# Optimization experiments

Measured on AMD Instinct MI355X. Metric: run time of the kernel, lower is better.

The kernel has to match this reference:

```python
import jax, jax.numpy as jnp
import numpy as np

N, E, DIM, H, T, R = 50000, 400000, 128, 8, 4, 6
D = DIM // H  # head dim = 16


def setup_inputs() -> dict:
    key = jax.random.key(0)
    ks = jax.random.split(key, 12)
    s = 0.1
    return {
        "x": jax.random.normal(ks[0], (N, DIM), jnp.float32),
        "src": jax.random.randint(ks[1], (E,), 0, N),
        "dst": jax.random.randint(ks[2], (E,), 0, N),
        "ntype": jax.random.randint(ks[3], (N,), 0, T),
        "etype": jax.random.randint(ks[4], (E,), 0, R),
        # TypedLinear weights: [num_types, in, out] (no bias in DGL TypedLinear)
        "Wk": jax.random.normal(ks[5], (T, DIM, DIM), jnp.float32) * s,
        "Wq": jax.random.normal(ks[6], (T, DIM, DIM), jnp.float32) * s,
        "Wv": jax.random.normal(ks[7], (T, DIM, DIM), jnp.float32) * s,
        "Wa": jax.random.normal(ks[8], (T, DIM, DIM), jnp.float32) * s,
        # relation_pri[h][r], relation_att/msg: per-head per-etype [D,D]
        "rel_pri": jnp.ones((H, R), jnp.float32) + jax.random.normal(ks[9], (H, R), jnp.float32) * 0.1,
        "rel_att": jax.random.normal(ks[10], (H, R, D, D), jnp.float32) * 0.25,
        "rel_msg": jax.random.normal(ks[11], (H, R, D, D), jnp.float32) * 0.25,
        "skip": jnp.ones((T,), jnp.float32),  # sigmoid-gated skip per node type
        "ln_gamma": jnp.ones((DIM,), jnp.float32),
        "ln_beta": jnp.zeros((DIM,), jnp.float32),
    }


def _typed_linear(x, W, types):
    # x: [N, in], W: [Ttypes, in, out], types: [N] -> y_i = x_i @ W[types_i]
    out = jnp.zeros((x.shape[0], W.shape[-1]), x.dtype)
    for t in range(W.shape[0]):
        out = jnp.where((types == t)[:, None], x @ W[t], out)
    return out


def _typed_rel(xe, W, etype):
    # xe: [E, H, D], W: [H, Rtypes, D, D] -> y_e[h] = xe_e[h] @ W[h, etype_e]
    out = jnp.zeros_like(xe)
    for r in range(W.shape[1]):
        yr = jnp.einsum('ehd,hdo->eho', xe, W[:, r])
        out = jnp.where((etype == r)[:, None, None], yr, out)
    return out


def reference(x, src, dst, ntype, etype, Wk, Wq, Wv, Wa, rel_pri, rel_att, rel_msg, skip, ln_gamma, ln_beta):
    # ---- HGTConv ----
    k = _typed_linear(x, Wk, ntype).reshape(N, H, D)
    q = _typed_linear(x, Wq, ntype).reshape(N, H, D)
    v = _typed_linear(x, Wv, ntype).reshape(N, H, D)
    k_e = k[src]   # [E,H,D]
    q_e = q[dst]
    v_e = v[src]
    kw = _typed_rel(k_e, rel_att, etype)                       # [E,H,D]
    a = (kw * q_e).sum(-1) * rel_pri.T[etype] / jnp.sqrt(jnp.float32(D))  # [E,H]
    m = _typed_rel(v_e, rel_msg, etype)                        # [E,H,D]
    # edge softmax over incoming edges per dst node, per head
    amax = jax.lax.stop_gradient(jax.ops.segment_max(a, dst, num_segments=N))
    amax = jnp.where(jnp.isfinite(amax), amax, 0.0)
    ex = jnp.exp(a - amax[dst])
    den = jax.ops.segment_sum(ex, dst, num_segments=N)
    attn = ex / jnp.maximum(den[dst], 1e-9)                    # [E,H]
    h = jax.ops.segment_sum(m * attn[:, :, None], dst, num_segments=N).reshape(N, DIM)
    h = _typed_linear(h, Wa, ntype)  # dropout = identity (eval mode)
    gate = jax.nn.sigmoid(skip)[ntype][:, None]
    h = h * gate + x * (1.0 - gate)  # in_dim == out_dim -> identity skip path
    # ---- RelationAwareLayer tail: Identity residual + dropout(identity) + LayerNorm ----
    y = x + h
    mu = y.mean(-1, keepdims=True)
    var = ((y - mu) ** 2).mean(-1, keepdims=True)
    return (y - mu) / jnp.sqrt(var + 1e-5) * ln_gamma + ln_beta
```

## Files before the change

kernel.cpp:

```cpp
#include <hip/hip_runtime.h>
#include <math.h>

#define N_NODES 50000
#define N_EDGES 400000
#define H_HEADS 8
#define D_HEAD 16
#define R_TYPES 6
#define T_TYPES 4
#define DIM 128
#define BN 16
#define MAX_TILES ((N_NODES + BN - 1) / BN + T_TYPES)
#define NKEYS (N_NODES * R_TYPES)
#define NBLK_K ((NKEYS + 255) / 256)
#define SM_SHIFT 8.0f
#define MAXB 16

typedef unsigned short bf16_t;

__device__ __forceinline__ float bf2f(bf16_t u) {
    unsigned int v = ((unsigned int)u) << 16;
    return __int_as_float((int)v);
}
__device__ __forceinline__ bf16_t f2bf(float f) {
    unsigned int u = (unsigned int)__float_as_int(f);
    unsigned int lsb = (u >> 16) & 1u;
    u += 0x7fffu + lsb;
    return (bf16_t)(u >> 16);
}
__device__ __forceinline__ void bf2x(unsigned int u, float& a, float& b) {
    a = bf2f((bf16_t)(u & 0xffffu));
    b = bf2f((bf16_t)(u >> 16));
}


__global__ void k_scanA(const int* __restrict__ cnt, int* __restrict__ offs,
                        int* __restrict__ partial, int n) {
    __shared__ int tmp[256];
    int tid = threadIdx.x;
    int i = blockIdx.x * 256 + tid;
    int v = (i < n) ? cnt[i] : 0;
    tmp[tid] = v;
    __syncthreads();
    for (int o = 1; o < 256; o <<= 1) {
        int t = (tid >= o) ? tmp[tid - o] : 0;
        __syncthreads();
        tmp[tid] += t;
        __syncthreads();
    }
    if (i < n) offs[i] = tmp[tid] - v;
    if (tid == 255) partial[blockIdx.x] = tmp[255];
}

__global__ void k_rscan(int* __restrict__ a, int total) {
    __shared__ int tmp[256];
    __shared__ int carry_s;
    int tid = threadIdx.x;
    if (tid == 0) carry_s = 0;
    __syncthreads();
    for (int base = 0; base < total; base += 256) {
        int i = base + tid;
        int v = (i < total) ? a[i] : 0;
        tmp[tid] = v;
        __syncthreads();
        for (int o = 1; o < 256; o <<= 1) {
            int t = (tid >= o) ? tmp[tid - o] : 0;
            __syncthreads();
            tmp[tid] += t;
            __syncthreads();
        }
        int carry = carry_s;
        if (i < total) a[i] = carry + tmp[tid] - v;
        __syncthreads();
        if (tid == 255) carry_s = carry + tmp[255];
        __syncthreads();
    }
}

__global__ void k_scanC2(int* __restrict__ offs, const int* __restrict__ partial,
                         int* __restrict__ cursor, int n) {
    int i = blockIdx.x * 256 + threadIdx.x;
    if (i < n) {
        int v = offs[i] + partial[blockIdx.x];
        offs[i] = v;
        cursor[i] = v;
    }
}


__global__ void k_count6(const int* __restrict__ dst, const int* __restrict__ etype,
                         int* __restrict__ deg6, int n) {
    int e = blockIdx.x * blockDim.x + threadIdx.x;
    if (e < n) atomicAdd(&deg6[etype[e] * N_NODES + dst[e]], 1);
}

__global__ void k_scatter6(const int* __restrict__ src, const int* __restrict__ dst,
                           const int* __restrict__ etype, int* __restrict__ cursor6,
                           int* __restrict__ esrc_s, int* __restrict__ edst_s, int n) {
    int e = blockIdx.x * blockDim.x + threadIdx.x;
    if (e < n) {
        int key = etype[e] * N_NODES + dst[e];
        int pos = atomicAdd(&cursor6[key], 1);
        esrc_s[pos] = src[e];
        edst_s[pos] = dst[e];
    }
}


__global__ void k_tcount_agg(const int* __restrict__ ntype, int* __restrict__ tcnt,
                             int* __restrict__ wpos, int n) {
    __shared__ int hist[T_TYPES];
    __shared__ int base[T_TYPES];
    int tid = threadIdx.x;
    if (tid < T_TYPES) hist[tid] = 0;
    __syncthreads();
    int i = blockIdx.x * 256 + tid;
    int t = 0, rank = 0;
    if (i < n) {
        t = ntype[i];
        rank = atomicAdd(&hist[t], 1);
    }
    __syncthreads();
    if (tid < T_TYPES)
        base[tid] = (hist[tid] > 0) ? atomicAdd(&tcnt[tid], hist[tid]) : 0;
    __syncthreads();
    if (i < n) wpos[i] = base[t] + rank;
}

__global__ void k_tsetup(const int* __restrict__ tcnt, int* __restrict__ pbase,
                         int* __restrict__ ntiles_g, int* __restrict__ tile_type) {
    __shared__ int off[T_TYPES + 1];
    if (threadIdx.x == 0) {
        int o = 0;
        for (int t = 0; t < T_TYPES; ++t) {
            off[t] = o;
            pbase[t] = o * BN;
            o += (tcnt[t] + BN - 1) / BN;
        }
        off[T_TYPES] = o;
        *ntiles_g = o;
    }
    __syncthreads();
    int total = off[T_TYPES];
    for (int i = threadIdx.x; i < total; i += blockDim.x) {
        int t = 0;
        while (t < T_TYPES - 1 && i >= off[t + 1]) ++t;
        tile_type[i] = t;
    }
}

__global__ void k_tscatter2(const int* __restrict__ ntype, const int* __restrict__ wpos,
                            const int* __restrict__ pbase, int* __restrict__ nlist, int n) {
    int i = blockIdx.x * 256 + threadIdx.x;
    if (i < n) nlist[pbase[ntype[i]] + wpos[i]] = i;
}


__global__ __launch_bounds__(192) void k_kqv_gemm4(
    const float* __restrict__ x, const int* __restrict__ nlist,
    const int* __restrict__ tile_type, const int* __restrict__ ntiles_g,
    const float* __restrict__ Wk, const float* __restrict__ Wq,
    const float* __restrict__ Wv,
    bf16_t* __restrict__ kb, bf16_t* __restrict__ qb, bf16_t* __restrict__ vb) {
    __shared__ float xs[BN][DIM];
    __shared__ int sids[BN];
    int b = blockIdx.x;
    if (b >= *ntiles_g) return;
    int tid = threadIdx.x;
    if (tid < BN) sids[tid] = nlist[b * BN + tid];
    __syncthreads();
    for (int idx = tid; idx < BN * (DIM / 4); idx += 192) {
        int row = idx >> 5;
        int q4 = idx & 31;
        int nid = sids[row];
        float4 v4 = make_float4(0.f, 0.f, 0.f, 0.f);
        if (nid >= 0) v4 = *(const float4*)(x + (size_t)nid * DIM + q4 * 4);
        *(float4*)(&xs[row][q4 * 4]) = v4;
    }
    __syncthreads();
    int lt = tid / 96;
    int wi = tid % 96;
    int mat = wi >> 5;
    int colq = wi & 31;
    int t = tile_type[b];
    const float* W = (mat == 0 ? Wk : (mat == 1 ? Wq : Wv))
                     + (size_t)t * DIM * DIM + colq * 4;
    float acc[8][4];
#pragma unroll
    for (int n = 0; n < 8; ++n) {
        acc[n][0] = 0.f; acc[n][1] = 0.f; acc[n][2] = 0.f; acc[n][3] = 0.f;
    }
    const float* xbase = &xs[lt * 8][0];
    for (int dq = 0; dq < 32; ++dq) {
        float4 w0 = *(const float4*)(W + (size_t)(dq * 4 + 0) * DIM);
        float4 w1 = *(const float4*)(W + (size_t)(dq * 4 + 1) * DIM);
        float4 w2 = *(const float4*)(W + (size_t)(dq * 4 + 2) * DIM);
        float4 w3 = *(const float4*)(W + (size_t)(dq * 4 + 3) * DIM);
#pragma unroll
        for (int n = 0; n < 8; ++n) {
            float4 xv = *(const float4*)(xbase + n * DIM + dq * 4);
            acc[n][0] = fmaf(xv.x, w0.x, acc[n][0]);
            acc[n][0] = fmaf(xv.y, w1.x, acc[n][0]);
            acc[n][0] = fmaf(xv.z, w2.x, acc[n][0]);
            acc[n][0] = fmaf(xv.w, w3.x, acc[n][0]);
            acc[n][1] = fmaf(xv.x, w0.y, acc[n][1]);
            acc[n][1] = fmaf(xv.y, w1.y, acc[n][1]);
            acc[n][1] = fmaf(xv.z, w2.y, acc[n][1]);
            acc[n][1] = fmaf(xv.w, w3.y, acc[n][1]);
            acc[n][2] = fmaf(xv.x, w0.z, acc[n][2]);
            acc[n][2] = fmaf(xv.y, w1.z, acc[n][2]);
            acc[n][2] = fmaf(xv.z, w2.z, acc[n][2]);
            acc[n][2] = fmaf(xv.w, w3.z, acc[n][2]);
            acc[n][3] = fmaf(xv.x, w0.w, acc[n][3]);
            acc[n][3] = fmaf(xv.y, w1.w, acc[n][3]);
            acc[n][3] = fmaf(xv.z, w2.w, acc[n][3]);
            acc[n][3] = fmaf(xv.w, w3.w, acc[n][3]);
        }
    }
    bf16_t* ob = (mat == 0 ? kb : (mat == 1 ? qb : vb));
#pragma unroll
    for (int n = 0; n < 8; ++n) {
        int nid = sids[lt * 8 + n];
        if (nid >= 0) {
            ushort4 o4;
            o4.x = f2bf(acc[n][0]); o4.y = f2bf(acc[n][1]);
            o4.z = f2bf(acc[n][2]); o4.w = f2bf(acc[n][3]);
            *(ushort4*)(ob + (size_t)nid * DIM + colq * 4) = o4;
        }
    }
}


__global__ __launch_bounds__(256) void k_edge_a4(
    const bf16_t* __restrict__ kbuf, const bf16_t* __restrict__ qbuf,
    const int* __restrict__ esrc_s, const int* __restrict__ edst_s,
    const int* __restrict__ beg6,
    const float* __restrict__ rel_att, const float* __restrict__ rel_pri,
    float* __restrict__ a_ws, int nE) {
    __shared__ float A2[2][8 * 260];
    __shared__ float pri[2][8];
    __shared__ int rb_s[R_TYPES + 1];
    __shared__ int r01[2];
    int b = blockIdx.x;
    int e0 = b * 32;
    int tid = threadIdx.x;
    int nHere = nE - e0; if (nHere > 32) nHere = 32;
    if (nHere <= 0) return;
    if (tid < R_TYPES) rb_s[tid] = beg6[tid * N_NODES];
    if (tid == R_TYPES) rb_s[R_TYPES] = nE;
    __syncthreads();
    if (tid == 0) {
        int rA = 0, rB = 0;
        int eL = e0 + nHere - 1;
#pragma unroll
        for (int r = 1; r < R_TYPES; ++r) {
            if (e0 >= rb_s[r]) rA = r;
            if (eL >= rb_s[r]) rB = r;
        }
        r01[0] = rA; r01[1] = rB;
    }
    __syncthreads();
    int r0 = r01[0], r1 = r01[1];
    int bnd = rb_s[r0 + 1];
    for (int idx = tid; idx < 2 * 2048; idx += 256) {
        int slot = idx >> 11;
        if (slot == 1 && r1 == r0) break;
        int rem = idx & 2047;
        int h = rem >> 8, dj = rem & 255;
        int rr = slot ? r1 : r0;
        A2[slot][h * 260 + dj] = rel_att[(h * R_TYPES + rr) * 256 + dj];
    }
    if (tid < 16) {
        int slot = tid >> 3, h = tid & 7;
        pri[slot][h] = rel_pri[h * R_TYPES + (slot ? r1 : r0)] * 0.25f;
    }
    __syncthreads();
    int el = tid >> 3;
    int h  = tid & 7;
    int q2 = e0 + el;
    if (q2 >= nE) return;
    int s = esrc_s[q2], dn = edst_s[q2];
    int slot = (q2 >= bnd) ? 1 : 0;
    const uint4* kp = (const uint4*)(kbuf + (size_t)s  * DIM + h * 16);
    const uint4* qp = (const uint4*)(qbuf + (size_t)dn * DIM + h * 16);
    uint4 ka = kp[0], kb4 = kp[1];
    uint4 qa = qp[0], qb4 = qp[1];
    float kk[16], qq[16];
    bf2x(ka.x,  kk[0],  kk[1]);  bf2x(ka.y,  kk[2],  kk[3]);
    bf2x(ka.z,  kk[4],  kk[5]);  bf2x(ka.w,  kk[6],  kk[7]);
    bf2x(kb4.x, kk[8],  kk[9]);  bf2x(kb4.y, kk[10], kk[11]);
    bf2x(kb4.z, kk[12], kk[13]); bf2x(kb4.w, kk[14], kk[15]);
    bf2x(qa.x,  qq[0],  qq[1]);  bf2x(qa.y,  qq[2],  qq[3]);
    bf2x(qa.z,  qq[4],  qq[5]);  bf2x(qa.w,  qq[6],  qq[7]);
    bf2x(qb4.x, qq[8],  qq[9]);  bf2x(qb4.y, qq[10], qq[11]);
    bf2x(qb4.z, qq[12], qq[13]); bf2x(qb4.w, qq[14], qq[15]);
    const float4* A4 = (const float4*)&A2[slot][h * 260];
    float accj[16];
#pragma unroll
    for (int j = 0; j < 16; ++j) accj[j] = 0.f;
#pragma unroll
    for (int d = 0; d < 16; ++d) {
        float kd = kk[d];
#pragma unroll
        for (int jj = 0; jj < 4; ++jj) {
            float4 a4 = A4[d * 4 + jj];
            accj[jj * 4 + 0] = fmaf(kd, a4.x, accj[jj * 4 + 0]);
            accj[jj * 4 + 1] = fmaf(kd, a4.y, accj[jj * 4 + 1]);
            accj[jj * 4 + 2] = fmaf(kd, a4.z, accj[jj * 4 + 2]);
            accj[jj * 4 + 3] = fmaf(kd, a4.w, accj[jj * 4 + 3]);
        }
    }
    float acc = 0.f;
#pragma unroll
    for (int j = 0; j < 16; ++j) acc = fmaf(accj[j], qq[j], acc);
    a_ws[(size_t)q2 * 8 + h] = acc * pri[slot][h];
}


__global__ __launch_bounds__(256) void k_aggregate10(
    const bf16_t* __restrict__ vbuf, const float* __restrict__ a_ws,
    const int* __restrict__ beg6, const int* __restrict__ esrc_s,
    const float* __restrict__ rel_msg,
    float* __restrict__ hacc, int n, int nE) {
    __shared__ float wsum[2][R_TYPES * 128];
    __shared__ float exl[2][MAXB][H_HEADS];
    __shared__ int   sl[2][MAXB];
    __shared__ int   rl[2][MAXB];
    __shared__ int   bb[2][2 * R_TYPES];
    __shared__ int   cum[2][R_TYPES + 1];
    __shared__ int   dgmax_s;
    int tid = threadIdx.x;
    int nb = tid >> 7;
    int lane2 = tid & 127;
    int node = blockIdx.x * 2 + nb;
    bool valid = node < n;
    int h = lane2 >> 4;
    int d = lane2 & 15;
    if (lane2 < 2 * R_TYPES) {
        int rr = lane2 >= R_TYPES ? lane2 - R_TYPES : lane2;
        int key = rr * N_NODES + (valid ? node : 0);
        int val;
        if (lane2 < R_TYPES) val = valid ? beg6[key] : 0;
        else                 val = valid ? ((key + 1 < NKEYS) ? beg6[key + 1] : nE) : 0;
        bb[nb][lane2] = val;
    }
    if (tid == 0) dgmax_s = 0;
    __syncthreads();
    if (lane2 == 0) {
        int c = 0;
#pragma unroll
        for (int rr = 0; rr < R_TYPES; ++rr) {
            cum[nb][rr] = c;
            c += bb[nb][R_TYPES + rr] - bb[nb][rr];
        }
        cum[nb][R_TYPES] = c;
        atomicMax(&dgmax_s, c);
    }
    __syncthreads();
    int dg = cum[nb][R_TYPES];
    int dgmax = dgmax_s;

    float* wsn = &wsum[nb][0];
#pragma unroll
    for (int rr = 0; rr < R_TYPES; ++rr) wsn[rr * 128 + lane2] = 0.f;

    float den = 0.f;
    float racc = 0.f;
    int rcur = -1;
    int js = lane2 >> 3;
    int hs = lane2 & 7;

    for (int base = 0; base < dgmax; base += MAXB) {
        __syncthreads();
        int jj = base + js;
        if (jj < dg) {
            int rr = 0;
#pragma unroll
            for (int q = 1; q < R_TYPES; ++q) if (jj >= cum[nb][q]) rr = q;
            int p = bb[nb][rr] + (jj - cum[nb][rr]);
            exl[nb][js][hs] = __expf(a_ws[(size_t)p * 8 + hs] - SM_SHIFT);
            if (hs == 0) { sl[nb][js] = esrc_s[p]; rl[nb][js] = rr; }
        }
        __syncthreads();
        int cnt = dg - base; if (cnt > MAXB) cnt = MAXB; if (cnt < 0) cnt = 0;
#pragma unroll 4
        for (int j = 0; j < cnt; ++j) {
            int r = rl[nb][j];
            if (r != rcur) {
                if (rcur >= 0) wsn[rcur * 128 + lane2] += racc;
                racc = 0.f;
                rcur = r;
            }
            float ex = exl[nb][j][h];
            den += ex;
            float vv = bf2f(vbuf[(size_t)sl[nb][j] * DIM + lane2]);
            racc = fmaf(ex, vv, racc);
        }
    }
    if (rcur >= 0) wsn[rcur * 128 + lane2] += racc;
    __syncthreads();

    float acc = 0.f;
#pragma unroll
    for (int rr = 0; rr < R_TYPES; ++rr) {
        const float*  M   = rel_msg + ((size_t)h * R_TYPES + rr) * 256;
        const float4* blr = (const float4*)&wsn[rr * 128 + h * 16];
#pragma unroll
        for (int dq = 0; dq < 4; ++dq) {
            float4 bv = blr[dq];
            acc = fmaf(bv.x, M[(dq * 4 + 0) * 16 + d], acc);
            acc = fmaf(bv.y, M[(dq * 4 + 1) * 16 + d], acc);
            acc = fmaf(bv.z, M[(dq * 4 + 2) * 16 + d], acc);
            acc = fmaf(bv.w, M[(dq * 4 + 3) * 16 + d], acc);
        }
    }
    if (valid)
        hacc[(size_t)node * DIM + lane2] = acc / fmaxf(den, 1e-9f);
}


__global__ __launch_bounds__(256) void k_final_gemm(
    const float* __restrict__ x, const int* __restrict__ nlist,
    const int* __restrict__ tile_type, const int* __restrict__ ntiles_g,
    const float* __restrict__ Wa, const float* __restrict__ skip,
    const float* __restrict__ gamma, const float* __restrict__ beta,
    float* __restrict__ out) {
    __shared__ float hs[BN][DIM];
    __shared__ float ys[BN][DIM];
    __shared__ int sids[BN];
    __shared__ float mred[BN], ired[BN];
    int b = blockIdx.x;
    if (b >= *ntiles_g) return;
    int tid = threadIdx.x;
    if (tid < BN) sids[tid] = nlist[b * BN + tid];
    __syncthreads();
    for (int idx = tid; idx < BN * DIM; idx += 256) {
        int row = idx >> 7, col = idx & 127;
        int nid = sids[row];
        hs[row][col] = (nid >= 0) ? out[(size_t)nid * DIM + col] : 0.f;
    }
    __syncthreads();
    int t = tile_type[b];
    int half = tid >> 7, col = tid & 127;
    const float* W = Wa + (size_t)t * DIM * DIM;
    float acc[8];
#pragma unroll
    for (int n = 0; n < 8; ++n) acc[n] = 0.f;
#pragma unroll 4
    for (int d = 0; d < DIM; ++d) {
        float w = W[d * DIM + col];
#pragma unroll
        for (int n = 0; n < 8; ++n) acc[n] = fmaf(hs[half * 8 + n][d], w, acc[n]);
    }
    float gte = 1.f / (1.f + __expf(-skip[t]));
#pragma unroll
    for (int n = 0; n < 8; ++n) {
        int row = half * 8 + n;
        int nid = sids[row];
        float xv = (nid >= 0) ? x[(size_t)nid * DIM + col] : 0.f;
        ys[row][col] = xv * (2.f - gte) + acc[n] * gte;
    }
    __syncthreads();
    int ng = tid >> 4, l16 = tid & 15;
    float s = 0.f, s2 = 0.f;
#pragma unroll
    for (int k2 = 0; k2 < 8; ++k2) {
        float yv = ys[ng][l16 + 16 * k2];
        s += yv; s2 += yv * yv;
    }
#pragma unroll
    for (int m = 1; m < 16; m <<= 1) {
        s  += __shfl_xor(s, m, 64);
        s2 += __shfl_xor(s2, m, 64);
    }
    if (l16 == 0) {
        float mu = s * (1.f / DIM);
        float var = s2 * (1.f / DIM) - mu * mu;
        mred[ng] = mu;
        ired[ng] = rsqrtf(var + 1e-5f);
    }
    __syncthreads();
    float gm = gamma[col], bt = beta[col];
#pragma unroll
    for (int n = 0; n < 8; ++n) {
        int row = half * 8 + n;
        int nid = sids[row];
        if (nid >= 0)
            out[(size_t)nid * DIM + col] = (ys[row][col] - mred[row]) * ired[row] * gm + bt;
    }
}


extern "C" void kernel_launch(void* const* d_in, const int* in_sizes, int n_in,
                              void* d_out, int out_size, void* d_ws, size_t ws_size,
                              hipStream_t stream) {
    const float* x       = (const float*)d_in[0];
    const int*   src     = (const int*)d_in[1];
    const int*   dst     = (const int*)d_in[2];
    const int*   ntype   = (const int*)d_in[3];
    const int*   etype   = (const int*)d_in[4];
    const float* Wk      = (const float*)d_in[5];
    const float* Wq      = (const float*)d_in[6];
    const float* Wv      = (const float*)d_in[7];
    const float* Wa      = (const float*)d_in[8];
    const float* rel_pri = (const float*)d_in[9];
    const float* rel_att = (const float*)d_in[10];
    const float* rel_msg = (const float*)d_in[11];
    const float* skip    = (const float*)d_in[12];
    const float* gamma   = (const float*)d_in[13];
    const float* beta    = (const float*)d_in[14];
    float* out = (float*)d_out;

    const int N = N_NODES, E = N_EDGES;

    char* ws = (char*)d_ws;
    float* a_ws = (float*)ws;
    int* deg6    = (int*)(a_ws + (size_t)E * H_HEADS);
    int* beg6    = deg6 + NKEYS;
    int* cursor6 = beg6 + NKEYS;
    int* partial6 = cursor6 + NKEYS;
    int* esrc_s  = partial6 + NBLK_K;
    int* edst_s  = esrc_s + E;
    int* tcnt    = edst_s + E;
    int* pbase   = tcnt + T_TYPES;
    int* ntiles  = pbase + T_TYPES;
    int* tile_type = ntiles + 1;
    int* nlist   = tile_type + MAX_TILES;
    int* wpos    = nlist + (size_t)MAX_TILES * BN;
    bf16_t* kb   = (bf16_t*)(wpos + N);
    bf16_t* qb   = kb + (size_t)N * DIM;
    bf16_t* vb   = qb + (size_t)N * DIM;

    const int nbScan = (N + 255) / 256;

    hipMemsetAsync(deg6, 0, (size_t)NKEYS * sizeof(int), stream);
    k_count6<<<(E + 255) / 256, 256, 0, stream>>>(dst, etype, deg6, E);
    k_scanA<<<NBLK_K, 256, 0, stream>>>(deg6, beg6, partial6, NKEYS);
    k_rscan<<<1, 256, 0, stream>>>(partial6, NBLK_K);
    k_scanC2<<<NBLK_K, 256, 0, stream>>>(beg6, partial6, cursor6, NKEYS);
    k_scatter6<<<(E + 255) / 256, 256, 0, stream>>>(
        src, dst, etype, cursor6, esrc_s, edst_s, E);

    hipMemsetAsync(tcnt, 0, T_TYPES * sizeof(int), stream);
    k_tcount_agg<<<nbScan, 256, 0, stream>>>(ntype, tcnt, wpos, N);
    k_tsetup<<<1, 256, 0, stream>>>(tcnt, pbase, ntiles, tile_type);
    hipMemsetAsync(nlist, 0xFF, (size_t)MAX_TILES * BN * sizeof(int), stream);
    k_tscatter2<<<nbScan, 256, 0, stream>>>(ntype, wpos, pbase, nlist, N);

    k_kqv_gemm4<<<MAX_TILES, 192, 0, stream>>>(
        x, nlist, tile_type, ntiles, Wk, Wq, Wv, kb, qb, vb);

    k_edge_a4<<<(E + 31) / 32, 256, 0, stream>>>(
        kb, qb, esrc_s, edst_s, beg6, rel_att, rel_pri, a_ws, E);

    k_aggregate10<<<(N + 1) / 2, 256, 0, stream>>>(
        vb, a_ws, beg6, esrc_s, rel_msg, out, N, E);

    k_final_gemm<<<MAX_TILES, 256, 0, stream>>>(
        x, nlist, tile_type, ntiles, Wa, skip, gamma, beta, out);
}
```

Measured before the change: 386.5 us.

## Compute per-edge messages in edge kernel and stream-aggregate by destination order

The edge kernel now also gathers V, applies the per-relation message matrix per edge, computes exp(score) and writes exp-weighted bf16 messages into a buffer ordered by destination, using a new per-destination CSR (count, scan, dpos atomics). Aggregation becomes a contiguous streaming sum per node with no per-relation grouping or shared-memory matrix multiply. This drops the gather of V in aggregation and the per-node rel_msg product. In exchange it does E×H×D message FLOPs instead of N×R, writes and rereads a large bf16 message buffer, rounds messages to bf16 before summing, and adds extra preprocessing kernels.

```diff
diff --git a/kernel.cpp b/kernel.cpp
--- a/kernel.cpp
+++ b/kernel.cpp
@@ -12,8 +12,8 @@
 #define MAX_TILES ((N_NODES + BN - 1) / BN + T_TYPES)
 #define NKEYS (N_NODES * R_TYPES)
 #define NBLK_K ((NKEYS + 255) / 256)
+#define NBLK_N ((N_NODES + 255) / 256)
 #define SM_SHIFT 8.0f
-#define MAXB 16
 
 typedef unsigned short bf16_t;
 
@@ -30,6 +30,9 @@
 __device__ __forceinline__ void bf2x(unsigned int u, float& a, float& b) {
     a = bf2f((bf16_t)(u & 0xffffu));
     b = bf2f((bf16_t)(u >> 16));
+}
+__device__ __forceinline__ unsigned int pk(float a, float b) {
+    return (unsigned int)f2bf(a) | ((unsigned int)f2bf(b) << 16);
 }
 
 
@@ -93,6 +96,11 @@
     if (e < n) atomicAdd(&deg6[etype[e] * N_NODES + dst[e]], 1);
 }
 
+__global__ void k_countD(const int* __restrict__ dst, int* __restrict__ degD, int n) {
+    int e = blockIdx.x * blockDim.x + threadIdx.x;
+    if (e < n) atomicAdd(&degD[dst[e]], 1);
+}
+
 __global__ void k_scatter6(const int* __restrict__ src, const int* __restrict__ dst,
                            const int* __restrict__ etype, int* __restrict__ cursor6,
                            int* __restrict__ esrc_s, int* __restrict__ edst_s, int n) {
@@ -103,6 +111,12 @@
         esrc_s[pos] = src[e];
         edst_s[pos] = dst[e];
     }
+}
+
+__global__ void k_dpos(const int* __restrict__ edst_s, int* __restrict__ cursorD,
+                       int* __restrict__ dpos, int n) {
+    int p = blockIdx.x * blockDim.x + threadIdx.x;
+    if (p < n) dpos[p] = atomicAdd(&cursorD[edst_s[p]], 1);
 }
 
 
@@ -230,13 +244,16 @@
 }
 
 
-__global__ __launch_bounds__(256) void k_edge_a4(
+__global__ __launch_bounds__(256) void k_edge_m(
     const bf16_t* __restrict__ kbuf, const bf16_t* __restrict__ qbuf,
+    const bf16_t* __restrict__ vbuf,
     const int* __restrict__ esrc_s, const int* __restrict__ edst_s,
-    const int* __restrict__ beg6,
-    const float* __restrict__ rel_att, const float* __restrict__ rel_pri,
-    float* __restrict__ a_ws, int nE) {
+    const int* __restrict__ beg6, const int* __restrict__ dpos,
+    const float* __restrict__ rel_att, const float* __restrict__ rel_msg,
+    const float* __restrict__ rel_pri,
+    float* __restrict__ ex_out, bf16_t* __restrict__ m_out, int nE) {
     __shared__ float A2[2][8 * 260];
+    __shared__ float M2[2][8 * 260];
     __shared__ float pri[2][8];
     __shared__ int rb_s[R_TYPES + 1];
     __shared__ int r01[2];
@@ -268,6 +285,7 @@
         int h = rem >> 8, dj = rem & 255;
         int rr = slot ? r1 : r0;
         A2[slot][h * 260 + dj] = rel_att[(h * R_TYPES + rr) * 256 + dj];
+        M2[slot][h * 260 + dj] = rel_msg[(h * R_TYPES + rr) * 256 + dj];
     }
     if (tid < 16) {
         int slot = tid >> 3, h = tid & 7;
@@ -282,9 +300,11 @@
     int slot = (q2 >= bnd) ? 1 : 0;
     const uint4* kp = (const uint4*)(kbuf + (size_t)s  * DIM + h * 16);
     const uint4* qp = (const uint4*)(qbuf + (size_t)dn * DIM + h * 16);
+    const uint4* vp = (const uint4*)(vbuf + (size_t)s  * DIM + h * 16);
     uint4 ka = kp[0], kb4 = kp[1];
     uint4 qa = qp[0], qb4 = qp[1];
-    float kk[16], qq[16];
+    uint4 va = vp[0], vb4 = vp[1];
+    float kk[16], qq[16], vv[16];
     bf2x(ka.x,  kk[0],  kk[1]);  bf2x(ka.y,  kk[2],  kk[3]);
     bf2x(ka.z,  kk[4],  kk[5]);  bf2x(ka.w,  kk[6],  kk[7]);
     bf2x(kb4.x, kk[8],  kk[9]);  bf2x(kb4.y, kk[10], kk[11]);
@@ -293,6 +313,11 @@
     bf2x(qa.z,  qq[4],  qq[5]);  bf2x(qa.w,  qq[6],  qq[7]);
     bf2x(qb4.x, qq[8],  qq[9]);  bf2x(qb4.y, qq[10], qq[11]);
     bf2x(qb4.z, qq[12], qq[13]); bf2x(qb4.w, qq[14], qq[15]);
+    bf2x(va.x,  vv[0],  vv[1]);  bf2x(va.y,  vv[2],  vv[3]);
+    bf2x(va.z,  vv[4],  vv[5]);  bf2x(va.w,  vv[6],  vv[7]);
+    bf2x(vb4.x, vv[8],  vv[9]);  bf2x(vb4.y, vv[10], vv[11]);
+    bf2x(vb4.z, vv[12], vv[13]); bf2x(vb4.w, vv[14], vv[15]);
+
     const float4* A4 = (const float4*)&A2[slot][h * 260];
     float accj[16];
 #pragma unroll
@@ -309,112 +334,58 @@
             accj[jj * 4 + 3] = fmaf(kd, a4.w, accj[jj * 4 + 3]);
         }
     }
-    float acc = 0.f;
-#pragma unroll
-    for (int j = 0; j < 16; ++j) acc = fmaf(accj[j], qq[j], acc);
-    a_ws[(size_t)q2 * 8 + h] = acc * pri[slot][h];
-}
-
-
-__global__ __launch_bounds__(256) void k_aggregate10(
-    const bf16_t* __restrict__ vbuf, const float* __restrict__ a_ws,
-    const int* __restrict__ beg6, const int* __restrict__ esrc_s,
-    const float* __restrict__ rel_msg,
-    float* __restrict__ hacc, int n, int nE) {
-    __shared__ float wsum[2][R_TYPES * 128];
-    __shared__ float exl[2][MAXB][H_HEADS];
-    __shared__ int   sl[2][MAXB];
-    __shared__ int   rl[2][MAXB];
-    __shared__ int   bb[2][2 * R_TYPES];
-    __shared__ int   cum[2][R_TYPES + 1];
-    __shared__ int   dgmax_s;
+    float a = 0.f;
+#pragma unroll
+    for (int j = 0; j < 16; ++j) a = fmaf(accj[j], qq[j], a);
+    float ex = __expf(a * pri[slot][h] - SM_SHIFT);
+
+    const float4* M4 = (const float4*)&M2[slot][h * 260];
+    float mj[16];
+#pragma unroll
+    for (int j = 0; j < 16; ++j) mj[j] = 0.f;
+#pragma unroll
+    for (int d = 0; d < 16; ++d) {
+        float vd = vv[d];
+#pragma unroll
+        for (int jj = 0; jj < 4; ++jj) {
+            float4 m4 = M4[d * 4 + jj];
+            mj[jj * 4 + 0] = fmaf(vd, m4.x, mj[jj * 4 + 0]);
+            mj[jj * 4 + 1] = fmaf(vd, m4.y, mj[jj * 4 + 1]);
+            mj[jj * 4 + 2] = fmaf(vd, m4.z, mj[jj * 4 + 2]);
+            mj[jj * 4 + 3] = fmaf(vd, m4.w, mj[jj * 4 + 3]);
+        }
+    }
+    int dp = dpos[q2];
+    ex_out[(size_t)dp * 8 + h] = ex;
+    uint4 o0, o1;
+    o0.x = pk(ex * mj[0],  ex * mj[1]);  o0.y = pk(ex * mj[2],  ex * mj[3]);
+    o0.z = pk(ex * mj[4],  ex * mj[5]);  o0.w = pk(ex * mj[6],  ex * mj[7]);
+    o1.x = pk(ex * mj[8],  ex * mj[9]);  o1.y = pk(ex * mj[10], ex * mj[11]);
+    o1.z = pk(ex * mj[12], ex * mj[13]); o1.w = pk(ex * mj[14], ex * mj[15]);
+    uint4* op = (uint4*)(m_out + (size_t)dp * DIM + h * 16);
+    op[0] = o0; op[1] = o1;
+}
+
+
+__global__ __launch_bounds__(256) void k_agg_stream(
+    const bf16_t* __restrict__ m_out, const float* __restrict__ ex_out,
+    const int* __restrict__ doffD, const int* __restrict__ degD,
+    float* __restrict__ hacc, int n) {
     int tid = threadIdx.x;
     int nb = tid >> 7;
     int lane2 = tid & 127;
     int node = blockIdx.x * 2 + nb;
-    bool valid = node < n;
+    if (node >= n) return;
     int h = lane2 >> 4;
-    int d = lane2 & 15;
-    if (lane2 < 2 * R_TYPES) {
-        int rr = lane2 >= R_TYPES ? lane2 - R_TYPES : lane2;
-        int key = rr * N_NODES + (valid ? node : 0);
-        int val;
-        if (lane2 < R_TYPES) val = valid ? beg6[key] : 0;
-        else                 val = valid ? ((key + 1 < NKEYS) ? beg6[key + 1] : nE) : 0;
-        bb[nb][lane2] = val;
-    }
-    if (tid == 0) dgmax_s = 0;
-    __syncthreads();
-    if (lane2 == 0) {
-        int c = 0;
-#pragma unroll
-        for (int rr = 0; rr < R_TYPES; ++rr) {
-            cum[nb][rr] = c;
-            c += bb[nb][R_TYPES + rr] - bb[nb][rr];
-        }
-        cum[nb][R_TYPES] = c;
-        atomicMax(&dgmax_s, c);
-    }
-    __syncthreads();
-    int dg = cum[nb][R_TYPES];
-    int dgmax = dgmax_s;
-
-    float* wsn = &wsum[nb][0];
-#pragma unroll
-    for (int rr = 0; rr < R_TYPES; ++rr) wsn[rr * 128 + lane2] = 0.f;
-
-    float den = 0.f;
-    float racc = 0.f;
-    int rcur = -1;
-    int js = lane2 >> 3;
-    int hs = lane2 & 7;
-
-    for (int base = 0; base < dgmax; base += MAXB) {
-        __syncthreads();
-        int jj = base + js;
-        if (jj < dg) {
-            int rr = 0;
-#pragma unroll
-            for (int q = 1; q < R_TYPES; ++q) if (jj >= cum[nb][q]) rr = q;
-            int p = bb[nb][rr] + (jj - cum[nb][rr]);
-            exl[nb][js][hs] = __expf(a_ws[(size_t)p * 8 + hs] - SM_SHIFT);
-            if (hs == 0) { sl[nb][js] = esrc_s[p]; rl[nb][js] = rr; }
-        }
-        __syncthreads();
-        int cnt = dg - base; if (cnt > MAXB) cnt = MAXB; if (cnt < 0) cnt = 0;
+    int off = doffD[node];
+    int dg  = degD[node];
+    float acc = 0.f, den = 0.f;
 #pragma unroll 4
-        for (int j = 0; j < cnt; ++j) {
-            int r = rl[nb][j];
-            if (r != rcur) {
-                if (rcur >= 0) wsn[rcur * 128 + lane2] += racc;
-                racc = 0.f;
-                rcur = r;
-            }
-            float ex = exl[nb][j][h];
-            den += ex;
-            float vv = bf2f(vbuf[(size_t)sl[nb][j] * DIM + lane2]);
-            racc = fmaf(ex, vv, racc);
-        }
-    }
-    if (rcur >= 0) wsn[rcur * 128 + lane2] += racc;
-    __syncthreads();
-
-    float acc = 0.f;
-#pragma unroll
-    for (int rr = 0; rr < R_TYPES; ++rr) {
-        const float*  M   = rel_msg + ((size_t)h * R_TYPES + rr) * 256;
-        const float4* blr = (const float4*)&wsn[rr * 128 + h * 16];
-#pragma unroll
-        for (int dq = 0; dq < 4; ++dq) {
-            float4 bv = blr[dq];
-            acc = fmaf(bv.x, M[(dq * 4 + 0) * 16 + d], acc);
-            acc = fmaf(bv.y, M[(dq * 4 + 1) * 16 + d], acc);
-            acc = fmaf(bv.z, M[(dq * 4 + 2) * 16 + d], acc);
-            acc = fmaf(bv.w, M[(dq * 4 + 3) * 16 + d], acc);
-        }
-    }
-    if (valid)
-        hacc[(size_t)node * DIM + lane2] = acc / fmaxf(den, 1e-9f);
+    for (int j = 0; j < dg; ++j) {
+        den += ex_out[(size_t)(off + j) * 8 + h];
+        acc += bf2f(m_out[(size_t)(off + j) * DIM + lane2]);
+    }
+    hacc[(size_t)node * DIM + lane2] = acc / fmaxf(den, 1e-9f);
 }
 
 
@@ -513,12 +484,17 @@
     const int N = N_NODES, E = N_EDGES;
 
     char* ws = (char*)d_ws;
-    float* a_ws = (float*)ws;
-    int* deg6    = (int*)(a_ws + (size_t)E * H_HEADS);
+    float* ex_out = (float*)ws;
+    int* deg6    = (int*)(ex_out + (size_t)E * H_HEADS);
     int* beg6    = deg6 + NKEYS;
     int* cursor6 = beg6 + NKEYS;
     int* partial6 = cursor6 + NKEYS;
-    int* esrc_s  = partial6 + NBLK_K;
+    int* degD    = partial6 + NBLK_K;
+    int* doffD   = degD + N;
+    int* cursorD = doffD + N;
+    int* partialD = cursorD + N;
+    int* dpos    = partialD + NBLK_N;
+    int* esrc_s  = dpos + E;
     int* edst_s  = esrc_s + E;
     int* tcnt    = edst_s + E;
     int* pbase   = tcnt + T_TYPES;
@@ -529,31 +505,39 @@
     bf16_t* kb   = (bf16_t*)(wpos + N);
     bf16_t* qb   = kb + (size_t)N * DIM;
     bf16_t* vb   = qb + (size_t)N * DIM;
-
-    const int nbScan = (N + 255) / 256;
+    bf16_t* m_out = vb + (size_t)N * DIM;
+
+    const int nbE = (E + 255) / 256;
 
     hipMemsetAsync(deg6, 0, (size_t)NKEYS * sizeof(int), stream);
-    k_count6<<<(E + 255) / 256, 256, 0, stream>>>(dst, etype, deg6, E);
+    hipMemsetAsync(degD, 0, (size_t)N * sizeof(int), stream);
+    k_count6<<<nbE, 256, 0, stream>>>(dst, etype, deg6, E);
+    k_countD<<<nbE, 256, 0, stream>>>(dst, degD, E);
     k_scanA<<<NBLK_K, 256, 0, stream>>>(deg6, beg6, partial6, NKEYS);
     k_rscan<<<1, 256, 0, stream>>>(partial6, NBLK_K);
     k_scanC2<<<NBLK_K, 256, 0, stream>>>(beg6, partial6, cursor6, NKEYS);
-    k_scatter6<<<(E + 255) / 256, 256, 0, stream>>>(
+    k_scanA<<<NBLK_N, 256, 0, stream>>>(degD, doffD, partialD, N);
+    k_rscan<<<1, 256, 0, stream>>>(partialD, NBLK_N);
+    k_scanC2<<<NBLK_N, 256, 0, stream>>>(doffD, partialD, cursorD, N);
+    k_scatter6<<<nbE, 256, 0, stream>>>(
         src, dst, etype, cursor6, esrc_s, edst_s, E);
+    k_dpos<<<nbE, 256, 0, stream>>>(edst_s, cursorD, dpos, E);
 
     hipMemsetAsync(tcnt, 0, T_TYPES * sizeof(int), stream);
-    k_tcount_agg<<<nbScan, 256, 0, stream>>>(ntype, tcnt, wpos, N);
+    k_tcount_agg<<<NBLK_N, 256, 0, stream>>>(ntype, tcnt, wpos, N);
     k_tsetup<<<1, 256, 0, stream>>>(tcnt, pbase, ntiles, tile_type);
     hipMemsetAsync(nlist, 0xFF, (size_t)MAX_TILES * BN * sizeof(int), stream);
-    k_tscatter2<<<nbScan, 256, 0, stream>>>(ntype, wpos, pbase, nlist, N);
+    k_tscatter2<<<NBLK_N, 256, 0, stream>>>(ntype, wpos, pbase, nlist, N);
 
     k_kqv_gemm4<<<MAX_TILES, 192, 0, stream>>>(
         x, nlist, tile_type, ntiles, Wk, Wq, Wv, kb, qb, vb);
 
-    k_edge_a4<<<(E + 31) / 32, 256, 0, stream>>>(
-        kb, qb, esrc_s, edst_s, beg6, rel_att, rel_pri, a_ws, E);
-
-    k_aggregate10<<<(N + 1) / 2, 256, 0, stream>>>(
-        vb, a_ws, beg6, esrc_s, rel_msg, out, N, E);
+    k_edge_m<<<(E + 31) / 32, 256, 0, stream>>>(
+        kb, qb, vb, esrc_s, edst_s, beg6, dpos,
+        rel_att, rel_msg, rel_pri, ex_out, m_out, E);
+
+    k_agg_stream<<<(N + 1) / 2, 256, 0, stream>>>(
+        m_out, ex_out, doffD, degD, out, N);
 
     k_final_gemm<<<MAX_TILES, 256, 0, stream>>>(
         x, nlist, tile_type, ntiles, Wa, skip, gamma, beta, out);
```

After: 384.9 us. Within noise of the previous version (-0.4%).
